# Kernel optimization log

Measured on AMD Instinct MI355X. Metric: run time of the kernel, lower is better.

The kernel has to match this reference:

```python
import jax, jax.numpy as jnp
import numpy as np

H = 2048       # hidden_size
NH = 16        # num_attention_heads
NKV = 4        # num_key_value_heads
HD = H // NH   # head_dim = 128
INTER = 8192   # intermediate_size
L = 2048       # packed sequence length
EPS = 1e-6


def rmsnorm(x, w, eps=EPS):
    var = jnp.mean(x * x, axis=-1, keepdims=True)
    return x * jax.lax.rsqrt(var + eps) * w


def setup_inputs() -> dict:
    key = jax.random.key(0)
    ks = jax.random.split(key, 9)
    s = 0.02
    return {
        "hidden_states": jax.random.normal(ks[0], (1, L, H), jnp.float32),
        "cu_seqlens_q": jnp.array([0, 512, 1280, 2048], jnp.int32),
        "ln1_w": jnp.ones((H,), jnp.float32),
        "ln2_w": jnp.ones((H,), jnp.float32),
        "q_w": jax.random.normal(ks[1], (NH * HD, H), jnp.float32) * s,
        "k_w": jax.random.normal(ks[2], (NKV * HD, H), jnp.float32) * s,
        "v_w": jax.random.normal(ks[3], (NKV * HD, H), jnp.float32) * s,
        "o_w": jax.random.normal(ks[4], (H, NH * HD), jnp.float32) * s,
        "gate_w": jax.random.normal(ks[5], (INTER, H), jnp.float32) * s,
        "up_w": jax.random.normal(ks[6], (INTER, H), jnp.float32) * s,
        "down_w": jax.random.normal(ks[7], (H, INTER), jnp.float32) * s,
    }


def _segment_mask(cu, q_len):
    # segment id of each position: repeat_interleave of arange over lengths
    pos = jnp.arange(q_len)
    seg = jnp.searchsorted(cu[1:], pos, side="right")  # [L]
    mask = seg[:, None] == seg[None, :]
    mask = mask & (pos[None, :] <= pos[:, None])  # causal, q_len == k_len
    return mask  # [L, L] bool


def _forward(hidden_states, cu_seqlens_q, ln1_w, ln2_w, q_w, k_w, v_w, o_w,
             gate_w, up_w, down_w):
    b, q_len, _ = hidden_states.shape
    residual = hidden_states
    normed = rmsnorm(hidden_states, ln1_w)

    # project_kv
    key_states = (normed @ k_w.T).reshape(b, q_len, NKV, HD)
    value_states = (normed @ v_w.T).reshape(b, q_len, NKV, HD)

    q = (normed @ q_w.T).reshape(b, q_len, NH, HD)
    rep = NH // NKV
    k = jnp.repeat(key_states, rep, axis=2)   # repeat_interleave over heads
    v = jnp.repeat(value_states, rep, axis=2)

    scores = jnp.einsum("bqhd,bkhd->bhqk", q, k) / np.sqrt(HD)
    mask = _segment_mask(cu_seqlens_q, q_len)
    scores = jnp.where(mask[None, None, :, :], scores,
                       jnp.finfo(scores.dtype).min)
    probs = jax.nn.softmax(scores.astype(jnp.float32), axis=-1).astype(q.dtype)
    attn = jnp.einsum("bhqk,bkhd->bqhd", probs, v).reshape(b, q_len, NH * HD)
    mixed = attn @ o_w.T

    hidden = residual + mixed
    residual = hidden
    normed2 = rmsnorm(hidden, ln2_w)
    mlp = (jax.nn.silu(normed2 @ gate_w.T) * (normed2 @ up_w.T)) @ down_w.T
    hidden = residual + mlp
    return hidden, key_states, value_states


def reference(hidden_states, cu_seqlens_q, ln1_w, ln2_w, q_w, k_w, v_w, o_w,
              gate_w, up_w, down_w):
    return _forward(hidden_states, cu_seqlens_q, ln1_w, ln2_w, q_w, k_w, v_w,
                    o_w, gate_w, up_w, down_w)
```

## Files before the change

### kernel.cpp

```cpp
#include <hip/hip_runtime.h>
#include <stdint.h>

typedef __bf16 bf16;
typedef __bf16 bf16x8 __attribute__((ext_vector_type(8)));
typedef float f32x4 __attribute__((ext_vector_type(4)));

#define L_SEQ 2048
#define H_DIM 2048
#define KV_DIM 512
#define QKV_LD 3072
#define INTER_DIM 8192

__device__ __forceinline__ void load_lds16(const void* g, void* l) {
  __builtin_amdgcn_global_load_lds(
      (const __attribute__((address_space(1))) void*)g,
      (__attribute__((address_space(3))) void*)l, 16, 0, 0);
}

__global__ __launch_bounds__(256)
void cvt_all(const float* __restrict__ q, const float* __restrict__ k,
             const float* __restrict__ v, const float* __restrict__ o,
             const float* __restrict__ g, const float* __restrict__ u,
             const float* __restrict__ dn, bf16* __restrict__ WB) {
  const int b = blockIdx.x;
  const float* s;
  size_t doff;
  int lb;
  if (b < 2048)       { s = q;  doff = 0;        lb = b; }
  else if (b < 2560)  { s = k;  doff = 4194304;  lb = b - 2048; }
  else if (b < 3072)  { s = v;  doff = 5242880;  lb = b - 2560; }
  else if (b < 5120)  { s = o;  doff = 6291456;  lb = b - 3072; }
  else if (b < 13312) { s = g;  doff = 10485760; lb = b - 5120; }
  else if (b < 21504) { s = u;  doff = 27262976; lb = b - 13312; }
  else                { s = dn; doff = 44040192; lb = b - 21504; }
  const size_t i = (size_t)lb * 2048 + threadIdx.x * 8;
  float4 a = *(const float4*)(s + i);
  float4 c = *(const float4*)(s + i + 4);
  bf16x8 ov;
  ov[0] = (bf16)a.x; ov[1] = (bf16)a.y; ov[2] = (bf16)a.z; ov[3] = (bf16)a.w;
  ov[4] = (bf16)c.x; ov[5] = (bf16)c.y; ov[6] = (bf16)c.z; ov[7] = (bf16)c.w;
  *(bf16x8*)(WB + doff + i) = ov;
}

__global__ __launch_bounds__(256)
void rmsnorm_bf16(const float* __restrict__ x, const float* __restrict__ w,
                  bf16* __restrict__ out) {
  const int row = blockIdx.x;
  const int t = threadIdx.x;
  const float* xr = x + (size_t)row * H_DIM + t * 8;
  float4 a = *(const float4*)xr;
  float4 b = *(const float4*)(xr + 4);
  float ss = a.x * a.x + a.y * a.y + a.z * a.z + a.w * a.w +
             b.x * b.x + b.y * b.y + b.z * b.z + b.w * b.w;
#pragma unroll
  for (int off = 1; off < 64; off <<= 1) ss += __shfl_xor(ss, off, 64);
  __shared__ float red[4];
  if ((t & 63) == 0) red[t >> 6] = ss;
  __syncthreads();
  ss = red[0] + red[1] + red[2] + red[3];
  const float rs = rsqrtf(ss * (1.0f / H_DIM) + 1e-6f);
  float4 w1 = *(const float4*)(w + t * 8);
  float4 w2 = *(const float4*)(w + t * 8 + 4);
  bf16x8 o;
  o[0] = (bf16)(a.x * rs * w1.x);
  o[1] = (bf16)(a.y * rs * w1.y);
  o[2] = (bf16)(a.z * rs * w1.z);
  o[3] = (bf16)(a.w * rs * w1.w);
  o[4] = (bf16)(b.x * rs * w2.x);
  o[5] = (bf16)(b.y * rs * w2.y);
  o[6] = (bf16)(b.z * rs * w2.z);
  o[7] = (bf16)(b.w * rs * w2.w);
  *(bf16x8*)(out + (size_t)row * H_DIM + t * 8) = o;
}

__global__ __launch_bounds__(256)
void add_rmsnorm(const float* __restrict__ p0, const float* __restrict__ p1,
                 const float* __restrict__ res, const float* __restrict__ w,
                 float* __restrict__ hidden, bf16* __restrict__ normed) {
  const int row = blockIdx.x;
  const int t = threadIdx.x;
  const size_t base = (size_t)row * H_DIM + t * 8;
  float4 a0 = *(const float4*)(p0 + base);
  float4 a1 = *(const float4*)(p0 + base + 4);
  float4 b0 = *(const float4*)(p1 + base);
  float4 b1 = *(const float4*)(p1 + base + 4);
  float4 c0 = *(const float4*)(res + base);
  float4 c1 = *(const float4*)(res + base + 4);
  float4 h0, h1;
  h0.x = a0.x + b0.x + c0.x; h0.y = a0.y + b0.y + c0.y;
  h0.z = a0.z + b0.z + c0.z; h0.w = a0.w + b0.w + c0.w;
  h1.x = a1.x + b1.x + c1.x; h1.y = a1.y + b1.y + c1.y;
  h1.z = a1.z + b1.z + c1.z; h1.w = a1.w + b1.w + c1.w;
  *(float4*)(hidden + base) = h0;
  *(float4*)(hidden + base + 4) = h1;
  float ss = h0.x * h0.x + h0.y * h0.y + h0.z * h0.z + h0.w * h0.w +
             h1.x * h1.x + h1.y * h1.y + h1.z * h1.z + h1.w * h1.w;
#pragma unroll
  for (int off = 1; off < 64; off <<= 1) ss += __shfl_xor(ss, off, 64);
  __shared__ float red[4];
  if ((t & 63) == 0) red[t >> 6] = ss;
  __syncthreads();
  ss = red[0] + red[1] + red[2] + red[3];
  const float rs = rsqrtf(ss * (1.0f / H_DIM) + 1e-6f);
  float4 w1 = *(const float4*)(w + t * 8);
  float4 w2 = *(const float4*)(w + t * 8 + 4);
  bf16x8 o;
  o[0] = (bf16)(h0.x * rs * w1.x);
  o[1] = (bf16)(h0.y * rs * w1.y);
  o[2] = (bf16)(h0.z * rs * w1.z);
  o[3] = (bf16)(h0.w * rs * w1.w);
  o[4] = (bf16)(h1.x * rs * w2.x);
  o[5] = (bf16)(h1.y * rs * w2.y);
  o[6] = (bf16)(h1.z * rs * w2.z);
  o[7] = (bf16)(h1.w * rs * w2.w);
  *(bf16x8*)(normed + (size_t)row * H_DIM + t * 8) = o;
}

__global__ __launch_bounds__(256)
void reduce_add4(const float* __restrict__ p, size_t zs,
                 const float* __restrict__ res, float* __restrict__ out) {
  const size_t i = ((size_t)blockIdx.x * 256 + threadIdx.x) * 4;
  float4 a = *(const float4*)(p + i);
  float4 b = *(const float4*)(p + zs + i);
  float4 c = *(const float4*)(p + 2 * zs + i);
  float4 d = *(const float4*)(p + 3 * zs + i);
  float4 r = *(const float4*)(res + i);
  float4 o;
  o.x = a.x + b.x + c.x + d.x + r.x;
  o.y = a.y + b.y + c.y + d.y + r.y;
  o.z = a.z + b.z + c.z + d.z + r.z;
  o.w = a.w + b.w + c.w + d.w + r.w;
  *(float4*)(out + i) = o;
}

enum { M_PART = 0, M_QKV = 1 };

template <int MODE>
__global__ __launch_bounds__(256, 2)
void gemm_bt(const bf16* __restrict__ A, int lda,
             const bf16* __restrict__ B, int ldb, int kpb,
             bf16* __restrict__ outb,
             float* __restrict__ outf, int ldof, size_t zstride,
             float* __restrict__ outk, float* __restrict__ outv) {
  __shared__ bf16 sA[128 * 32];
  __shared__ bf16 sB[128 * 32];
  const int t = threadIdx.x;
  const int lane = t & 63;
  const int l15 = lane & 15, l4 = lane >> 4;
  const int wm = ((t >> 6) >> 1) * 64;
  const int wn = ((t >> 6) & 1) * 64;
  const int m0 = blockIdx.y * 128;
  const int n0 = blockIdx.x * 128;
  const int kbeg = blockIdx.z * kpb;
  const int kend = kbeg + kpb;

  const f32x4 zero = {0.f, 0.f, 0.f, 0.f};
  f32x4 acc[4][4];
#pragma unroll
  for (int i = 0; i < 4; ++i)
#pragma unroll
    for (int j = 0; j < 4; ++j) acc[i][j] = zero;

  for (int k0 = kbeg; k0 < kend; k0 += 32) {
#pragma unroll
    for (int i = 0; i < 2; ++i) {
      const int flat = i * 4096 + t * 16;
      const int r = flat >> 6, cb = (flat & 63) >> 1;
      load_lds16(A + (size_t)(m0 + r) * lda + k0 + cb, (char*)sA + flat);
      load_lds16(B + (size_t)(n0 + r) * ldb + k0 + cb, (char*)sB + flat);
    }
    __syncthreads();

    bf16x8 af[4], bfr[4];
#pragma unroll
    for (int mi = 0; mi < 4; ++mi)
      af[mi] = *(const bf16x8*)(&sA[(wm + mi * 16 + l15) * 32 + l4 * 8]);
#pragma unroll
    for (int ni = 0; ni < 4; ++ni)
      bfr[ni] = *(const bf16x8*)(&sB[(wn + ni * 16 + l15) * 32 + l4 * 8]);
#pragma unroll
    for (int mi = 0; mi < 4; ++mi)
#pragma unroll
      for (int ni = 0; ni < 4; ++ni)
        acc[mi][ni] = __builtin_amdgcn_mfma_f32_16x16x32_bf16(
            af[mi], bfr[ni], acc[mi][ni], 0, 0, 0);
    __syncthreads();
  }

#pragma unroll
  for (int mi = 0; mi < 4; ++mi) {
#pragma unroll
    for (int ni = 0; ni < 4; ++ni) {
      const int row0 = m0 + wm + mi * 16 + l4 * 4;
      const int col = n0 + wn + ni * 16 + l15;
#pragma unroll
      for (int r = 0; r < 4; ++r) {
        const float c = acc[mi][ni][r];
        const size_t m = (size_t)(row0 + r);
        if (MODE == M_PART) {
          outf[zstride * blockIdx.z + m * ldof + col] = c;
        } else {
          outb[m * QKV_LD + col] = (bf16)c;
          if (col >= 2560)      outv[m * KV_DIM + (col - 2560)] = c;
          else if (col >= 2048) outk[m * KV_DIM + (col - 2048)] = c;
        }
      }
    }
  }
}

__global__ __launch_bounds__(256, 2)
void gemm_glu(const bf16* __restrict__ A, const bf16* __restrict__ Bg,
              const bf16* __restrict__ Bu, bf16* __restrict__ out) {
  __shared__ bf16 sA[128 * 32];
  __shared__ bf16 sG[128 * 32];
  __shared__ bf16 sU[128 * 32];
  const int t = threadIdx.x;
  const int lane = t & 63;
  const int l15 = lane & 15, l4 = lane >> 4;
  const int wm = ((t >> 6) >> 1) * 64;
  const int wn = ((t >> 6) & 1) * 64;
  const int m0 = blockIdx.y * 128;
  const int n0 = blockIdx.x * 128;

  const f32x4 zero = {0.f, 0.f, 0.f, 0.f};
  f32x4 ag[4][4], au[4][4];
#pragma unroll
  for (int i = 0; i < 4; ++i)
#pragma unroll
    for (int j = 0; j < 4; ++j) { ag[i][j] = zero; au[i][j] = zero; }

  for (int k0 = 0; k0 < H_DIM; k0 += 32) {
#pragma unroll
    for (int i = 0; i < 2; ++i) {
      const int flat = i * 4096 + t * 16;
      const int r = flat >> 6, cb = (flat & 63) >> 1;
      load_lds16(A + (size_t)(m0 + r) * H_DIM + k0 + cb, (char*)sA + flat);
      load_lds16(Bg + (size_t)(n0 + r) * H_DIM + k0 + cb, (char*)sG + flat);
      load_lds16(Bu + (size_t)(n0 + r) * H_DIM + k0 + cb, (char*)sU + flat);
    }
    __syncthreads();

    bf16x8 af[4], bg[4], bu[4];
#pragma unroll
    for (int mi = 0; mi < 4; ++mi)
      af[mi] = *(const bf16x8*)(&sA[(wm + mi * 16 + l15) * 32 + l4 * 8]);
#pragma unroll
    for (int ni = 0; ni < 4; ++ni) {
      bg[ni] = *(const bf16x8*)(&sG[(wn + ni * 16 + l15) * 32 + l4 * 8]);
      bu[ni] = *(const bf16x8*)(&sU[(wn + ni * 16 + l15) * 32 + l4 * 8]);
    }
#pragma unroll
    for (int mi = 0; mi < 4; ++mi)
#pragma unroll
      for (int ni = 0; ni < 4; ++ni) {
        ag[mi][ni] = __builtin_amdgcn_mfma_f32_16x16x32_bf16(
            af[mi], bg[ni], ag[mi][ni], 0, 0, 0);
        au[mi][ni] = __builtin_amdgcn_mfma_f32_16x16x32_bf16(
            af[mi], bu[ni], au[mi][ni], 0, 0, 0);
      }
    __syncthreads();
  }

#pragma unroll
  for (int mi = 0; mi < 4; ++mi) {
#pragma unroll
    for (int ni = 0; ni < 4; ++ni) {
      const int row0 = m0 + wm + mi * 16 + l4 * 4;
      const int col = n0 + wn + ni * 16 + l15;
#pragma unroll
      for (int r = 0; r < 4; ++r) {
        const float g = ag[mi][ni][r];
        const float u = au[mi][ni][r];
        const float s = g / (1.f + __expf(-g));
        out[(size_t)(row0 + r) * INTER_DIM + col] = (bf16)(s * u);
      }
    }
  }
}

__global__ __launch_bounds__(256, 2)
void attn_fwd(const bf16* __restrict__ qkv, const int* __restrict__ cu,
              bf16* __restrict__ out) {
  const int h = blockIdx.y;
  const int q0 = blockIdx.x * 64;
  const int kvh = h >> 2;
  const int t = threadIdx.x;
  const int lane = t & 63;
  const int w = t >> 6;
  const int l15 = lane & 15, l4 = lane >> 4;

  __shared__ bf16 sK[64 * 136];
  __shared__ bf16 sVt[128 * 72];
  __shared__ bf16 sP[4][16 * 64];

  const int c1 = cu[1], c2 = cu[2];
  const int seg0 = (q0 >= c2) ? c2 : ((q0 >= c1) ? c1 : 0);

  const int qrow = q0 + w * 16 + l15;
  bf16x8 qf[4];
#pragma unroll
  for (int kc = 0; kc < 4; ++kc) {
    bf16x8 v = *(const bf16x8*)(qkv + (size_t)qrow * QKV_LD + h * 128 +
                                kc * 32 + l4 * 8);
#pragma unroll
    for (int j = 0; j < 8; ++j)
      v[j] = (bf16)((float)v[j] * 0.08838834764831845f);
    qf[kc] = v;
  }

  const f32x4 zero = {0.f, 0.f, 0.f, 0.f};
  f32x4 oacc[8];
#pragma unroll
  for (int i = 0; i < 8; ++i) oacc[i] = zero;
  float mi[4] = {-1e30f, -1e30f, -1e30f, -1e30f};
  float li[4] = {0.f, 0.f, 0.f, 0.f};

  for (int k0 = seg0; k0 <= q0; k0 += 64) {
#pragma unroll
    for (int it = 0; it < 4; ++it) {
      const int flat = it * 4096 + t * 16;
      const int r = flat >> 8, db = flat & 255;
      *(bf16x8*)((char*)sK + r * 272 + db) = *(const bf16x8*)(
          (const char*)(qkv + (size_t)(k0 + r) * QKV_LD + 2048 + kvh * 128) +
          db);
      const int chunk = it * 256 + t;
      const int vr = chunk & 63, dc = chunk >> 6;
      bf16x8 vv = *(const bf16x8*)(qkv + (size_t)(k0 + vr) * QKV_LD + 2560 +
                                   kvh * 128 + dc * 8);
#pragma unroll
      for (int j = 0; j < 8; ++j) sVt[(dc * 8 + j) * 72 + vr] = vv[j];
    }
    __syncthreads();

    f32x4 sacc[4];
#pragma unroll
    for (int kg = 0; kg < 4; ++kg) {
      f32x4 a = zero;
#pragma unroll
      for (int kc = 0; kc < 4; ++kc) {
        bf16x8 kf = *(const bf16x8*)((const char*)sK + (kg * 16 + l15) * 272 +
                                     kc * 64 + l4 * 16);
        a = __builtin_amdgcn_mfma_f32_16x16x32_bf16(qf[kc], kf, a, 0, 0, 0);
      }
      sacc[kg] = a;
    }

    if (k0 == q0) {
#pragma unroll
      for (int kg = 0; kg < 4; ++kg) {
        const int kk = kg * 16 + l15;
#pragma unroll
        for (int r = 0; r < 4; ++r) {
          const int qq = w * 16 + l4 * 4 + r;
          if (kk > qq) sacc[kg][r] = -1e30f;
        }
      }
    }

    float mx[4], al[4], rs[4];
#pragma unroll
    for (int r = 0; r < 4; ++r)
      mx[r] = fmaxf(fmaxf(sacc[0][r], sacc[1][r]),
                    fmaxf(sacc[2][r], sacc[3][r]));
#pragma unroll
    for (int off = 1; off < 16; off <<= 1)
#pragma unroll
      for (int r = 0; r < 4; ++r)
        mx[r] = fmaxf(mx[r], __shfl_xor(mx[r], off, 64));
#pragma unroll
    for (int r = 0; r < 4; ++r) {
      const float mn = fmaxf(mi[r], mx[r]);
      al[r] = __expf(mi[r] - mn);
      mi[r] = mn;
      rs[r] = 0.f;
    }
#pragma unroll
    for (int kg = 0; kg < 4; ++kg)
#pragma unroll
      for (int r = 0; r < 4; ++r) {
        const float p = __expf(sacc[kg][r] - mi[r]);
        sacc[kg][r] = p;
        rs[r] += p;
      }
#pragma unroll
    for (int off = 1; off < 16; off <<= 1)
#pragma unroll
      for (int r = 0; r < 4; ++r) rs[r] += __shfl_xor(rs[r], off, 64);
#pragma unroll
    for (int r = 0; r < 4; ++r) li[r] = li[r] * al[r] + rs[r];
#pragma unroll
    for (int dn = 0; dn < 8; ++dn)
#pragma unroll
      for (int r = 0; r < 4; ++r) oacc[dn][r] *= al[r];

#pragma unroll
    for (int kg = 0; kg < 4; ++kg)
#pragma unroll
      for (int r = 0; r < 4; ++r)
        sP[w][(l4 * 4 + r) * 64 + kg * 16 + l15] = (bf16)sacc[kg][r];

    bf16x8 pf[2];
#pragma unroll
    for (int kc2 = 0; kc2 < 2; ++kc2)
      pf[kc2] = *(const bf16x8*)(&sP[w][l15 * 64 + kc2 * 32 + l4 * 8]);
#pragma unroll
    for (int dn = 0; dn < 8; ++dn)
#pragma unroll
      for (int kc2 = 0; kc2 < 2; ++kc2) {
        bf16x8 vf = *(const bf16x8*)(&sVt[(dn * 16 + l15) * 72 + kc2 * 32 +
                                          l4 * 8]);
        oacc[dn] = __builtin_amdgcn_mfma_f32_16x16x32_bf16(pf[kc2], vf,
                                                           oacc[dn], 0, 0, 0);
      }
    __syncthreads();
  }

#pragma unroll
  for (int dn = 0; dn < 8; ++dn)
#pragma unroll
    for (int r = 0; r < 4; ++r) {
      const size_t m = (size_t)(q0 + w * 16 + l4 * 4 + r);
      out[m * H_DIM + h * 128 + dn * 16 + l15] = (bf16)(oacc[dn][r] / li[r]);
    }
}

extern "C" void kernel_launch(void* const* d_in, const int* in_sizes, int n_in,
                              void* d_out, int out_size, void* d_ws,
                              size_t ws_size, hipStream_t stream) {
  (void)in_sizes; (void)n_in; (void)out_size; (void)ws_size;
  const float* hs     = (const float*)d_in[0];
  const int*   cu     = (const int*)d_in[1];
  const float* ln1    = (const float*)d_in[2];
  const float* ln2    = (const float*)d_in[3];
  const float* q_w    = (const float*)d_in[4];
  const float* k_w    = (const float*)d_in[5];
  const float* v_w    = (const float*)d_in[6];
  const float* o_w    = (const float*)d_in[7];
  const float* gate_w = (const float*)d_in[8];
  const float* up_w   = (const float*)d_in[9];
  const float* down_w = (const float*)d_in[10];

  float* out_hidden = (float*)d_out;
  float* out_k = out_hidden + (size_t)L_SEQ * H_DIM;
  float* out_v = out_k + (size_t)L_SEQ * KV_DIM;

  char* ws = (char*)d_ws;
  bf16* WB = (bf16*)ws;
  const size_t wq_off = 0;
  const size_t wo_off = 6291456;
  const size_t wg_off = 10485760;
  const size_t wu_off = 27262976;
  const size_t wd_off = 44040192;

  bf16*  normed1 = (bf16*)(ws + ((size_t)116 << 20));
  bf16*  qkv     = (bf16*)(ws + ((size_t)124 << 20));
  bf16*  attnb   = (bf16*)(ws + ((size_t)136 << 20));
  bf16*  normed2 = (bf16*)(ws + ((size_t)144 << 20));
  bf16*  interb  = (bf16*)(ws + ((size_t)152 << 20));
  float* opart   = (float*)(ws + ((size_t)152 << 20));
  float* dpart   = (float*)(ws + ((size_t)20 << 20));

  dim3 blk(256);

  cvt_all<<<29696, blk, 0, stream>>>(q_w, k_w, v_w, o_w, gate_w, up_w, down_w,
                                     WB);

  rmsnorm_bf16<<<L_SEQ, blk, 0, stream>>>(hs, ln1, normed1);

  gemm_bt<M_QKV><<<dim3(24, 16, 1), blk, 0, stream>>>(
      normed1, H_DIM, WB + wq_off, H_DIM, H_DIM, qkv, nullptr, 0, 0, out_k,
      out_v);

  attn_fwd<<<dim3(32, 16), blk, 0, stream>>>(qkv, cu, attnb);

  gemm_bt<M_PART><<<dim3(16, 16, 2), blk, 0, stream>>>(
      attnb, H_DIM, WB + wo_off, H_DIM, 1024, nullptr, opart, H_DIM,
      (size_t)L_SEQ * H_DIM, nullptr, nullptr);

  add_rmsnorm<<<L_SEQ, blk, 0, stream>>>(opart, opart + (size_t)L_SEQ * H_DIM,
                                         hs, ln2, out_hidden, normed2);

  gemm_glu<<<dim3(64, 16), blk, 0, stream>>>(normed2, WB + wg_off, WB + wu_off,
                                             interb);

  gemm_bt<M_PART><<<dim3(16, 16, 4), blk, 0, stream>>>(
      interb, INTER_DIM, WB + wd_off, INTER_DIM, 2048, nullptr, dpart, H_DIM,
      (size_t)L_SEQ * H_DIM, nullptr, nullptr);

  reduce_add4<<<4096, blk, 0, stream>>>(dpart, (size_t)L_SEQ * H_DIM,
                                        out_hidden, out_hidden);
}
```

Baseline: 665.0 us.

## Double GEMM k-step to 64 and split-K the QKV projection with a combine kernel

Both GEMM kernels now stage 64 columns of K per iteration instead of 32. This halves the number of barrier pairs and issues more loads per sync, at the cost of twice the shared memory per block. The QKV projection becomes a 2-way split-K GEMM writing fp32 partials. A new qkv_combine kernel sums them, writes the bf16 qkv buffer and the fp32 key/value outputs. gemm_bt's occupancy hint rises to 3 blocks per CU. This adds an extra launch and fp32 partial traffic in exchange for more blocks in flight on the QKV GEMM.

```diff
diff --git a/kernel.cpp b/kernel.cpp
--- a/kernel.cpp
+++ b/kernel.cpp
@@ -3,6 +3,7 @@
 
 typedef __bf16 bf16;
 typedef __bf16 bf16x8 __attribute__((ext_vector_type(8)));
+typedef __bf16 bf16x4v __attribute__((ext_vector_type(4)));
 typedef float f32x4 __attribute__((ext_vector_type(4)));
 
 #define L_SEQ 2048
@@ -133,17 +134,30 @@
   *(float4*)(out + i) = o;
 }
 
-enum { M_PART = 0, M_QKV = 1 };
-
-template <int MODE>
-__global__ __launch_bounds__(256, 2)
+__global__ __launch_bounds__(256)
+void qkv_combine(const float* __restrict__ p, size_t zs,
+                 bf16* __restrict__ qkv, float* __restrict__ outk,
+                 float* __restrict__ outv) {
+  const size_t i = ((size_t)blockIdx.x * 256 + threadIdx.x) * 4;
+  float4 a = *(const float4*)(p + i);
+  float4 b = *(const float4*)(p + zs + i);
+  float4 s;
+  s.x = a.x + b.x; s.y = a.y + b.y; s.z = a.z + b.z; s.w = a.w + b.w;
+  bf16x4v o;
+  o[0] = (bf16)s.x; o[1] = (bf16)s.y; o[2] = (bf16)s.z; o[3] = (bf16)s.w;
+  *(bf16x4v*)(qkv + i) = o;
+  const int col = (int)(i % QKV_LD);
+  const size_t row = i / QKV_LD;
+  if (col >= 2560)      *(float4*)(outv + row * KV_DIM + (col - 2560)) = s;
+  else if (col >= 2048) *(float4*)(outk + row * KV_DIM + (col - 2048)) = s;
+}
+
+__global__ __launch_bounds__(256, 3)
 void gemm_bt(const bf16* __restrict__ A, int lda,
              const bf16* __restrict__ B, int ldb, int kpb,
-             bf16* __restrict__ outb,
-             float* __restrict__ outf, int ldof, size_t zstride,
-             float* __restrict__ outk, float* __restrict__ outv) {
-  __shared__ bf16 sA[128 * 32];
-  __shared__ bf16 sB[128 * 32];
+             float* __restrict__ outf, int ldof, size_t zstride) {
+  __shared__ bf16 sA[2 * 128 * 32];
+  __shared__ bf16 sB[2 * 128 * 32];
   const int t = threadIdx.x;
   const int lane = t & 63;
   const int l15 = lane & 15, l4 = lane >> 4;
@@ -161,29 +175,37 @@
 #pragma unroll
     for (int j = 0; j < 4; ++j) acc[i][j] = zero;
 
-  for (int k0 = kbeg; k0 < kend; k0 += 32) {
-#pragma unroll
-    for (int i = 0; i < 2; ++i) {
+  for (int k0 = kbeg; k0 < kend; k0 += 64) {
+#pragma unroll
+    for (int i = 0; i < 4; ++i) {
       const int flat = i * 4096 + t * 16;
-      const int r = flat >> 6, cb = (flat & 63) >> 1;
-      load_lds16(A + (size_t)(m0 + r) * lda + k0 + cb, (char*)sA + flat);
-      load_lds16(B + (size_t)(n0 + r) * ldb + k0 + cb, (char*)sB + flat);
+      const int kc = flat >> 13;
+      const int wb = flat & 8191;
+      const int r = wb >> 6, ce = (wb & 63) >> 1;
+      const int gc = k0 + kc * 32 + ce;
+      load_lds16(A + (size_t)(m0 + r) * lda + gc, (char*)sA + flat);
+      load_lds16(B + (size_t)(n0 + r) * ldb + gc, (char*)sB + flat);
     }
     __syncthreads();
 
-    bf16x8 af[4], bfr[4];
-#pragma unroll
-    for (int mi = 0; mi < 4; ++mi)
-      af[mi] = *(const bf16x8*)(&sA[(wm + mi * 16 + l15) * 32 + l4 * 8]);
-#pragma unroll
-    for (int ni = 0; ni < 4; ++ni)
-      bfr[ni] = *(const bf16x8*)(&sB[(wn + ni * 16 + l15) * 32 + l4 * 8]);
-#pragma unroll
-    for (int mi = 0; mi < 4; ++mi)
+#pragma unroll
+    for (int kc = 0; kc < 2; ++kc) {
+      bf16x8 af[4], bfr[4];
+#pragma unroll
+      for (int mi = 0; mi < 4; ++mi)
+        af[mi] = *(const bf16x8*)(&sA[kc * 4096 + (wm + mi * 16 + l15) * 32 +
+                                      l4 * 8]);
 #pragma unroll
       for (int ni = 0; ni < 4; ++ni)
-        acc[mi][ni] = __builtin_amdgcn_mfma_f32_16x16x32_bf16(
-            af[mi], bfr[ni], acc[mi][ni], 0, 0, 0);
+        bfr[ni] = *(const bf16x8*)(&sB[kc * 4096 + (wn + ni * 16 + l15) * 32 +
+                                       l4 * 8]);
+#pragma unroll
+      for (int mi = 0; mi < 4; ++mi)
+#pragma unroll
+        for (int ni = 0; ni < 4; ++ni)
+          acc[mi][ni] = __builtin_amdgcn_mfma_f32_16x16x32_bf16(
+              af[mi], bfr[ni], acc[mi][ni], 0, 0, 0);
+    }
     __syncthreads();
   }
 
@@ -194,17 +216,9 @@
       const int row0 = m0 + wm + mi * 16 + l4 * 4;
       const int col = n0 + wn + ni * 16 + l15;
 #pragma unroll
-      for (int r = 0; r < 4; ++r) {
-        const float c = acc[mi][ni][r];
-        const size_t m = (size_t)(row0 + r);
-        if (MODE == M_PART) {
-          outf[zstride * blockIdx.z + m * ldof + col] = c;
-        } else {
-          outb[m * QKV_LD + col] = (bf16)c;
-          if (col >= 2560)      outv[m * KV_DIM + (col - 2560)] = c;
-          else if (col >= 2048) outk[m * KV_DIM + (col - 2048)] = c;
-        }
-      }
+      for (int r = 0; r < 4; ++r)
+        outf[zstride * blockIdx.z + (size_t)(row0 + r) * ldof + col] =
+            acc[mi][ni][r];
     }
   }
 }
@@ -212,9 +226,9 @@
 __global__ __launch_bounds__(256, 2)
 void gemm_glu(const bf16* __restrict__ A, const bf16* __restrict__ Bg,
               const bf16* __restrict__ Bu, bf16* __restrict__ out) {
-  __shared__ bf16 sA[128 * 32];
-  __shared__ bf16 sG[128 * 32];
-  __shared__ bf16 sU[128 * 32];
+  __shared__ bf16 sA[2 * 128 * 32];
+  __shared__ bf16 sG[2 * 128 * 32];
+  __shared__ bf16 sU[2 * 128 * 32];
   const int t = threadIdx.x;
   const int lane = t & 63;
   const int l15 = lane & 15, l4 = lane >> 4;
@@ -230,35 +244,44 @@
 #pragma unroll
     for (int j = 0; j < 4; ++j) { ag[i][j] = zero; au[i][j] = zero; }
 
-  for (int k0 = 0; k0 < H_DIM; k0 += 32) {
-#pragma unroll
-    for (int i = 0; i < 2; ++i) {
+  for (int k0 = 0; k0 < H_DIM; k0 += 64) {
+#pragma unroll
+    for (int i = 0; i < 4; ++i) {
       const int flat = i * 4096 + t * 16;
-      const int r = flat >> 6, cb = (flat & 63) >> 1;
-      load_lds16(A + (size_t)(m0 + r) * H_DIM + k0 + cb, (char*)sA + flat);
-      load_lds16(Bg + (size_t)(n0 + r) * H_DIM + k0 + cb, (char*)sG + flat);
-      load_lds16(Bu + (size_t)(n0 + r) * H_DIM + k0 + cb, (char*)sU + flat);
+      const int kc = flat >> 13;
+      const int wb = flat & 8191;
+      const int r = wb >> 6, ce = (wb & 63) >> 1;
+      const int gc = k0 + kc * 32 + ce;
+      load_lds16(A + (size_t)(m0 + r) * H_DIM + gc, (char*)sA + flat);
+      load_lds16(Bg + (size_t)(n0 + r) * H_DIM + gc, (char*)sG + flat);
+      load_lds16(Bu + (size_t)(n0 + r) * H_DIM + gc, (char*)sU + flat);
     }
     __syncthreads();
 
-    bf16x8 af[4], bg[4], bu[4];
-#pragma unroll
-    for (int mi = 0; mi < 4; ++mi)
-      af[mi] = *(const bf16x8*)(&sA[(wm + mi * 16 + l15) * 32 + l4 * 8]);
-#pragma unroll
-    for (int ni = 0; ni < 4; ++ni) {
-      bg[ni] = *(const bf16x8*)(&sG[(wn + ni * 16 + l15) * 32 + l4 * 8]);
-      bu[ni] = *(const bf16x8*)(&sU[(wn + ni * 16 + l15) * 32 + l4 * 8]);
-    }
-#pragma unroll
-    for (int mi = 0; mi < 4; ++mi)
+#pragma unroll
+    for (int kc = 0; kc < 2; ++kc) {
+      bf16x8 af[4], bg[4], bu[4];
+#pragma unroll
+      for (int mi = 0; mi < 4; ++mi)
+        af[mi] = *(const bf16x8*)(&sA[kc * 4096 + (wm + mi * 16 + l15) * 32 +
+                                      l4 * 8]);
 #pragma unroll
       for (int ni = 0; ni < 4; ++ni) {
-        ag[mi][ni] = __builtin_amdgcn_mfma_f32_16x16x32_bf16(
-            af[mi], bg[ni], ag[mi][ni], 0, 0, 0);
-        au[mi][ni] = __builtin_amdgcn_mfma_f32_16x16x32_bf16(
-            af[mi], bu[ni], au[mi][ni], 0, 0, 0);
+        bg[ni] = *(const bf16x8*)(&sG[kc * 4096 + (wn + ni * 16 + l15) * 32 +
+                                      l4 * 8]);
+        bu[ni] = *(const bf16x8*)(&sU[kc * 4096 + (wn + ni * 16 + l15) * 32 +
+                                      l4 * 8]);
       }
+#pragma unroll
+      for (int mi = 0; mi < 4; ++mi)
+#pragma unroll
+        for (int ni = 0; ni < 4; ++ni) {
+          ag[mi][ni] = __builtin_amdgcn_mfma_f32_16x16x32_bf16(
+              af[mi], bg[ni], ag[mi][ni], 0, 0, 0);
+          au[mi][ni] = __builtin_amdgcn_mfma_f32_16x16x32_bf16(
+              af[mi], bu[ni], au[mi][ni], 0, 0, 0);
+        }
+    }
     __syncthreads();
   }
 
@@ -458,8 +481,9 @@
   bf16*  attnb   = (bf16*)(ws + ((size_t)136 << 20));
   bf16*  normed2 = (bf16*)(ws + ((size_t)144 << 20));
   bf16*  interb  = (bf16*)(ws + ((size_t)152 << 20));
+  float* qpart   = (float*)(ws + ((size_t)136 << 20));
   float* opart   = (float*)(ws + ((size_t)152 << 20));
-  float* dpart   = (float*)(ws + ((size_t)20 << 20));
+  float* dpart   = (float*)(ws);
 
   dim3 blk(256);
 
@@ -468,15 +492,17 @@
 
   rmsnorm_bf16<<<L_SEQ, blk, 0, stream>>>(hs, ln1, normed1);
 
-  gemm_bt<M_QKV><<<dim3(24, 16, 1), blk, 0, stream>>>(
-      normed1, H_DIM, WB + wq_off, H_DIM, H_DIM, qkv, nullptr, 0, 0, out_k,
-      out_v);
+  gemm_bt<<<dim3(24, 16, 2), blk, 0, stream>>>(
+      normed1, H_DIM, WB + wq_off, H_DIM, 1024, qpart, QKV_LD,
+      (size_t)L_SEQ * QKV_LD);
+  qkv_combine<<<6144, blk, 0, stream>>>(qpart, (size_t)L_SEQ * QKV_LD, qkv,
+                                        out_k, out_v);
 
   attn_fwd<<<dim3(32, 16), blk, 0, stream>>>(qkv, cu, attnb);
 
-  gemm_bt<M_PART><<<dim3(16, 16, 2), blk, 0, stream>>>(
-      attnb, H_DIM, WB + wo_off, H_DIM, 1024, nullptr, opart, H_DIM,
-      (size_t)L_SEQ * H_DIM, nullptr, nullptr);
+  gemm_bt<<<dim3(16, 16, 2), blk, 0, stream>>>(
+      attnb, H_DIM, WB + wo_off, H_DIM, 1024, opart, H_DIM,
+      (size_t)L_SEQ * H_DIM);
 
   add_rmsnorm<<<L_SEQ, blk, 0, stream>>>(opart, opart + (size_t)L_SEQ * H_DIM,
                                          hs, ln2, out_hidden, normed2);
@@ -484,9 +510,9 @@
   gemm_glu<<<dim3(64, 16), blk, 0, stream>>>(normed2, WB + wg_off, WB + wu_off,
                                              interb);
 
-  gemm_bt<M_PART><<<dim3(16, 16, 4), blk, 0, stream>>>(
-      interb, INTER_DIM, WB + wd_off, INTER_DIM, 2048, nullptr, dpart, H_DIM,
-      (size_t)L_SEQ * H_DIM, nullptr, nullptr);
+  gemm_bt<<<dim3(16, 16, 4), blk, 0, stream>>>(
+      interb, INTER_DIM, WB + wd_off, INTER_DIM, 2048, dpart, H_DIM,
+      (size_t)L_SEQ * H_DIM);
 
   reduce_add4<<<4096, blk, 0, stream>>>(dpart, (size_t)L_SEQ * H_DIM,
                                         out_hidden, out_hidden);
```

Result: faster. 651.3 us (-2.1%).
